# Performance work log

Measured on AMD Instinct MI355X. Metric: run time of the kernel, lower is better.

The kernel has to match this reference:

```python
import jax, jax.numpy as jnp
import numpy as np

B, S, V, E, HE, HD, MEL_D, MEL_T = 4096, 13, 276, 128, 256, 256, 80, 250

def setup_inputs() -> dict:
    key = jax.random.key(0)
    ks = jax.random.split(key, 20)
    p = lambda k, sh: (jax.random.normal(k, sh, dtype=jnp.float32) * 0.05)
    return {
        'text': jax.random.randint(ks[0], (B, S), 0, V),
        'surprisal': jax.random.normal(ks[1], (B, S), dtype=jnp.float32),
        'emb': p(ks[2], (V, E)),
        'sw': p(ks[3], (E, 1)), 'sb': p(ks[4], (E,)),
        'ew_ih': p(ks[5], (4 * HE, E)), 'ew_hh': p(ks[6], (4 * HE, HE)),
        'eb_ih': p(ks[7], (4 * HE,)), 'eb_hh': p(ks[8], (4 * HE,)),
        'aw': p(ks[9], (1, HD + HE)), 'ab': p(ks[10], (1,)),
        'dw_ih': p(ks[11], (4 * HD, E + HE)), 'dw_hh': p(ks[12], (4 * HD, HD)),
        'db_ih': p(ks[13], (4 * HD,)), 'db_hh': p(ks[14], (4 * HD,)),
        'f1w': p(ks[15], (1024, S * HD)), 'f1b': p(ks[16], (1024,)),
        'f2w': p(ks[17], (MEL_D * MEL_T, 1024)), 'f2b': p(ks[18], (MEL_D * MEL_T,)),
        'init_in': jnp.zeros((E,), dtype=jnp.float32),
    }

def _lstm_cell(x, h, c, w_ih, w_hh, b_ih, b_hh, H):
    # PyTorch gate order: i, f, g, o
    g = x @ w_ih.T + b_ih + h @ w_hh.T + b_hh
    i, f, gg, o = jnp.split(g, 4, axis=-1)
    c2 = jax.nn.sigmoid(f) * c + jax.nn.sigmoid(i) * jnp.tanh(gg)
    h2 = jax.nn.sigmoid(o) * jnp.tanh(c2)
    return h2, c2

def reference(text, surprisal, emb, sw, sb, ew_ih, ew_hh, eb_ih, eb_hh,
              aw, ab, dw_ih, dw_hh, db_ih, db_hh, f1w, f1b, f2w, f2b, init_in):
    # embedding + surprisal projection
    x = emb[text] + (surprisal[..., None] @ sw.T + sb)  # [B,S,E]

    # encoder LSTM over time
    def enc_step(carry, xt):
        h, c = carry
        h2, c2 = _lstm_cell(xt, h, c, ew_ih, ew_hh, eb_ih, eb_hh, HE)
        return (h2, c2), h2
    h0 = jnp.zeros((B, HE), dtype=x.dtype)
    (h_n, c_n), enc_seq = jax.lax.scan(enc_step, (h0, h0), jnp.swapaxes(x, 0, 1))
    enc_out = jnp.swapaxes(enc_seq, 0, 1)  # [B,S,HE]

    # precompute encoder part of attention scores (constant across steps)
    aw_h, aw_e = aw[0, :HD], aw[0, HD:]
    enc_score = enc_out @ aw_e + ab[0]  # [B,S]

    dec_in = jnp.broadcast_to(init_in, (B, E))

    def dec_step(carry, _):
        h, c = carry
        scores = h @ aw_h + 0.0  # [B]
        w = jax.nn.softmax(scores[:, None] + enc_score, axis=1)  # [B,S]
        context = jnp.einsum('bs,bsh->bh', w, enc_out)
        xcat = jnp.concatenate([dec_in, context], axis=-1)
        h2, c2 = _lstm_cell(xcat, h, c, dw_ih, dw_hh, db_ih, db_hh, HD)
        return (h2, c2), h2
    _, dec_seq = jax.lax.scan(dec_step, (h_n, c_n), None, length=S)
    dec_out = jnp.swapaxes(dec_seq, 0, 1).reshape(B, S * HD)  # [B,13*256]

    hfc = jax.nn.relu(dec_out @ f1w.T + f1b)
    out = (hfc @ f2w.T + f2b).reshape(B, MEL_D, MEL_T)
    return out
```

## Files before the change

kernel.cpp:

```cpp
#include <hip/hip_runtime.h>
#include <hip/hip_bf16.h>
#include <stdint.h>
#include <stddef.h>

#define B 4096
#define S 13
#define NG 1024
#define MEL 20000
#define MELP 20224

typedef __attribute__((ext_vector_type(8))) short bf16x8;
typedef __attribute__((ext_vector_type(4))) float f32x4;

__device__ __forceinline__ void g2l16(void* lds, const void* g) {
    __builtin_amdgcn_global_load_lds(
        (const __attribute__((address_space(1))) void*)g,
        (__attribute__((address_space(3))) void*)lds, 16, 0, 0);
}

__device__ __forceinline__ float sigm(float x) { return 1.0f / (1.0f + expf(-x)); }
__device__ __forceinline__ float b2f(unsigned short u) {
    union { float f; unsigned int i; } x; x.i = ((unsigned)u) << 16; return x.f;
}
__device__ __forceinline__ unsigned short f2bu(float f) {
    __hip_bfloat16 h = __float2bfloat16(f);
    return *reinterpret_cast<unsigned short*>(&h);
}

__device__ __forceinline__ void swz_decode(int wg, int nwg, int nx, int& bx, int& by) {
    const int cpx = nwg >> 3;
    wg = (wg & 7) * cpx + (wg >> 3);
    const int gsz = nx * 4;
    const int grp = wg / gsz, rem = wg % gsz;
    by = grp * 4 + (rem & 3);
    bx = rem >> 2;
}

#define BAR() do { asm volatile("" ::: "memory"); \
    __builtin_amdgcn_s_barrier(); \
    __builtin_amdgcn_sched_barrier(0); } while (0)

#define P_DECL() \
    __shared__ __hip_bfloat16 As3[4][128 * 32]; \
    __shared__ __hip_bfloat16 Bs3[4][64 * 32]; \
    const int tid  = threadIdx.x; \
    const int lane = tid & 63; \
    const int wv   = tid >> 6; \
    const int l16  = lane & 15; \
    const int sr   = tid >> 2; \
    const int sc   = (((tid & 3) ^ ((tid >> 3) & 3)) << 3); \
    const int sl   = (((lane >> 4) ^ ((l16 >> 1) & 3)) << 3)

#define STG3(buf, k0) do { \
    g2l16(&As3[buf][sr * 32 + (tid & 3) * 8],         Ag + (size_t)sr * K + (k0) + sc); \
    g2l16(&As3[buf][(sr + 64) * 32 + (tid & 3) * 8],  Ag + (size_t)(sr + 64) * K + (k0) + sc); \
    g2l16(&Bs3[buf][sr * 32 + (tid & 3) * 8],         Wg + (size_t)sr * K + (k0) + sc); } while (0)

#define TILE3(cur, stg, k2, DO_STG) do { \
    const __hip_bfloat16* Ab = As3[cur]; \
    const __hip_bfloat16* Bb = Bs3[cur]; \
    bf16x8 af[2], bfr[4]; \
    _Pragma("unroll") for (int m = 0; m < 2; ++m) \
        af[m] = *(const bf16x8*)(Ab + (wv * 32 + m * 16 + l16) * 32 + sl); \
    _Pragma("unroll") for (int n = 0; n < 4; ++n) \
        bfr[n] = *(const bf16x8*)(Bb + (n * 16 + l16) * 32 + sl); \
    if (DO_STG) STG3(stg, k2); \
    __builtin_amdgcn_s_setprio(1); \
    _Pragma("unroll") for (int m = 0; m < 2; ++m) \
        _Pragma("unroll") for (int n = 0; n < 4; ++n) \
            acc[m][n] = __builtin_amdgcn_mfma_f32_16x16x32_bf16(af[m], bfr[n], acc[m][n], 0, 0, 0); \
    __builtin_amdgcn_s_setprio(0); \
} while (0)

#define PIPELINE(K) do { \
    const int nk = (K) >> 5; \
    STG3(0, 0); \
    STG3(1, 32); \
    STG3(2, 64); \
    asm volatile("s_waitcnt vmcnt(6)" ::: "memory"); \
    BAR(); \
    int cur = 0; \
    for (int t = 0; t < nk - 3; ++t) { \
        const int stg = (cur + 3) & 3; \
        TILE3(cur, stg, (t + 3) << 5, true); \
        asm volatile("s_waitcnt vmcnt(6)" ::: "memory"); \
        BAR(); \
        cur = (cur + 1) & 3; \
    } \
    TILE3(cur, 0, 0, false); \
    asm volatile("s_waitcnt vmcnt(3)" ::: "memory"); \
    BAR(); \
    cur = (cur + 1) & 3; \
    TILE3(cur, 0, 0, false); \
    asm volatile("s_waitcnt vmcnt(0)" ::: "memory"); \
    BAR(); \
    cur = (cur + 1) & 3; \
    TILE3(cur, 0, 0, false); \
} while (0)

__global__ __launch_bounds__(256, 2) void gemm3(
    const __hip_bfloat16* __restrict__ A,
    const __hip_bfloat16* __restrict__ W,
    const float* __restrict__ bias,
    float* __restrict__ Cf,
    __hip_bfloat16* __restrict__ Cbf,
    int N, int K, int ldc, int relu, int nx)
{
    P_DECL();
    int bx, by;
    swz_decode(blockIdx.x, gridDim.x, nx, bx, by);
    const int brow = by * 128, bcol = bx * 64;
    const __hip_bfloat16* Ag = A + (size_t)brow * K;
    const __hip_bfloat16* Wg = W + (size_t)bcol * K;
    f32x4 acc[2][4] = {};

    PIPELINE(K);

    const int r4 = (lane >> 4) * 4;
    #pragma unroll
    for (int m = 0; m < 2; ++m) {
        #pragma unroll
        for (int n = 0; n < 4; ++n) {
            const int col = bcol + n * 16 + l16;
            if (col >= N) continue;
            const float bv = bias ? bias[col] : 0.0f;
            #pragma unroll
            for (int r = 0; r < 4; ++r) {
                const int row = brow + wv * 32 + m * 16 + r4 + r;
                float v = acc[m][n][r] + bv;
                if (relu) v = v > 0.0f ? v : 0.0f;
                if (Cf)  Cf[(size_t)row * ldc + col] = v;
                if (Cbf) Cbf[(size_t)row * ldc + col] = __float2bfloat16(v);
            }
        }
    }
}

__global__ __launch_bounds__(256, 2) void gemm_lstm3(
    const __hip_bfloat16* __restrict__ A,
    const __hip_bfloat16* __restrict__ W,
    const float* __restrict__ bias,
    float* __restrict__ c,
    float* __restrict__ hf,
    __hip_bfloat16* __restrict__ hb1, int s1,
    __hip_bfloat16* __restrict__ hb2, int s2,
    int K)
{
    P_DECL();
    int bx, by;
    swz_decode(blockIdx.x, gridDim.x, 16, bx, by);
    const int brow = by * 128, bcol = bx * 64;
    const __hip_bfloat16* Ag = A + (size_t)brow * K;
    const __hip_bfloat16* Wg = W + (size_t)bcol * K;
    f32x4 acc[2][4] = {};

    PIPELINE(K);

    const int r4 = (lane >> 4) * 4;
    const int unit = bx * 16 + l16;
    const float b0 = bias[bcol + l16];
    const float b1 = bias[bcol + 16 + l16];
    const float b2 = bias[bcol + 32 + l16];
    const float b3 = bias[bcol + 48 + l16];
    #pragma unroll
    for (int m = 0; m < 2; ++m) {
        #pragma unroll
        for (int r = 0; r < 4; ++r) {
            const int row = brow + wv * 32 + m * 16 + r4 + r;
            const float gi = acc[m][0][r] + b0;
            const float gf = acc[m][1][r] + b1;
            const float gg = acc[m][2][r] + b2;
            const float go = acc[m][3][r] + b3;
            const size_t ci = (size_t)row * 256 + unit;
            const float c2 = sigm(gf) * c[ci] + sigm(gi) * tanhf(gg);
            const float h2 = sigm(go) * tanhf(c2);
            c[ci] = c2;
            if (hf) hf[ci] = h2;
            const __hip_bfloat16 hb = __float2bfloat16(h2);
            hb1[(size_t)row * s1 + unit] = hb;
            if (hb2) hb2[(size_t)row * s2 + unit] = hb;
        }
    }
}

__global__ __launch_bounds__(512, 2) void gemm256(
    const __hip_bfloat16* __restrict__ A,
    const __hip_bfloat16* __restrict__ W,
    const float* __restrict__ bias,
    float* __restrict__ Cf,
    int N, int K, int ldc, int nx)
{
    __shared__ __hip_bfloat16 As[4][256 * 32];
    __shared__ __hip_bfloat16 Bs[4][256 * 32];
    const int tid  = threadIdx.x;
    const int lane = tid & 63;
    const int wv = tid >> 6, wr = wv >> 2, wc = wv & 3;
    const int l16 = lane & 15;
    int bx, by;
    {
        int wg = blockIdx.x; const int nwg = gridDim.x;
        const int cpx = nwg >> 3;
        wg = (wg & 7) * cpx + (wg >> 3);
        const int gsz = nx * 2;
        const int grp = wg / gsz, rem = wg % gsz;
        by = grp * 2 + (rem & 1);
        bx = rem >> 1;
    }
    const int brow = by * 256, bcol = bx * 256;
    const __hip_bfloat16* Ag = A + (size_t)brow * K;
    const __hip_bfloat16* Wg = W + (size_t)bcol * K;
    const int sr = tid >> 2;
    const int sc = (((tid & 3) ^ ((tid >> 3) & 3)) << 3);
    const int sd = tid * 8;
    const int sl = (((lane >> 4) ^ ((l16 >> 1) & 3)) << 3);
    f32x4 acc[8][4] = {};
    const int nk = K >> 5;

    #define STG_A(buf, k0) do { \
        g2l16(&As[buf][sd],        Ag + (size_t)sr * K + (k0) + sc);         \
        g2l16(&As[buf][4096 + sd], Ag + (size_t)(sr + 128) * K + (k0) + sc); } while (0)
    #define STG_B(buf, k0) do { \
        g2l16(&Bs[buf][sd],        Wg + (size_t)sr * K + (k0) + sc);         \
        g2l16(&Bs[buf][4096 + sd], Wg + (size_t)(sr + 128) * K + (k0) + sc); } while (0)

    #define TILE(cur, stg, k2, DO_STG) do {                                    \
        const __hip_bfloat16* Ab = As[cur];                                    \
        const __hip_bfloat16* Bb = Bs[cur];                                    \
        bf16x8 bfr[4], af[4];                                                  \
        _Pragma("unroll") for (int n = 0; n < 4; ++n)                          \
            bfr[n] = *(const bf16x8*)(Bb + (wc * 64 + n * 16 + l16) * 32 + sl);\
        _Pragma("unroll") for (int m = 0; m < 4; ++m)                          \
            af[m] = *(const bf16x8*)(Ab + (wr * 128 + m * 16 + l16) * 32 + sl);\
        if (DO_STG) STG_A(stg, k2);                                            \
        BAR();                                                                 \
        __builtin_amdgcn_s_setprio(1);                                         \
        _Pragma("unroll") for (int m = 0; m < 4; ++m)                          \
            _Pragma("unroll") for (int n = 0; n < 4; ++n)                      \
                acc[m][n] = __builtin_amdgcn_mfma_f32_16x16x32_bf16(           \
                    af[m], bfr[n], acc[m][n], 0, 0, 0);                        \
        __builtin_amdgcn_s_setprio(0);                                         \
        BAR();                                                                 \
        _Pragma("unroll") for (int m = 0; m < 4; ++m)                          \
            af[m] = *(const bf16x8*)(Ab + (wr * 128 + (m + 4) * 16 + l16) * 32 + sl); \
        if (DO_STG) STG_B(stg, k2);                                            \
        BAR();                                                                 \
        __builtin_amdgcn_s_setprio(1);                                         \
        _Pragma("unroll") for (int m = 0; m < 4; ++m)                          \
            _Pragma("unroll") for (int n = 0; n < 4; ++n)                      \
                acc[m + 4][n] = __builtin_amdgcn_mfma_f32_16x16x32_bf16(       \
                    af[m], bfr[n], acc[m + 4][n], 0, 0, 0);                    \
        __builtin_amdgcn_s_setprio(0);                                         \
    } while (0)

    STG_A(0, 0);  STG_B(0, 0);
    STG_A(1, 32); STG_B(1, 32);
    STG_A(2, 64); STG_B(2, 64);
    asm volatile("s_waitcnt vmcnt(8)" ::: "memory");
    BAR();
    int cur = 0;
    for (int t = 0; t < nk - 3; ++t) {
        const int stg = (cur + 3) & 3;
        TILE(cur, stg, (t + 3) << 5, true);
        asm volatile("s_waitcnt vmcnt(8)" ::: "memory");
        BAR();
        cur = (cur + 1) & 3;
    }
    TILE(cur, 0, 0, false);
    asm volatile("s_waitcnt vmcnt(4)" ::: "memory");
    BAR();
    cur = (cur + 1) & 3;
    TILE(cur, 0, 0, false);
    asm volatile("s_waitcnt vmcnt(0)" ::: "memory");
    BAR();
    cur = (cur + 1) & 3;
    TILE(cur, 0, 0, false);

    const int r4 = (lane >> 4) * 4;
    #pragma unroll
    for (int m = 0; m < 8; ++m) {
        #pragma unroll
        for (int n = 0; n < 4; ++n) {
            const int col = bcol + wc * 64 + n * 16 + l16;
            if (col >= N) continue;
            const float bv = bias[col];
            #pragma unroll
            for (int r = 0; r < 4; ++r) {
                const int row = brow + wr * 128 + m * 16 + r4 + r;
                Cf[(size_t)row * ldc + col] = acc[m][n][r] + bv;
            }
        }
    }
}

__device__ __forceinline__ int unperm(int np) {
    const int u = ((np >> 6) << 4) + (np & 15);
    const int g = (np >> 4) & 3;
    return g * 256 + u;
}

__global__ void pack_enc_w(const float* __restrict__ ew_ih, const float* __restrict__ ew_hh,
                           __hip_bfloat16* __restrict__ out) {
    int idx = blockIdx.x * 256 + threadIdx.x;
    if (idx >= NG * 384) return;
    int np = idx / 384, k = idx % 384;
    int n = unperm(np);
    float v = (k < 128) ? ew_ih[n * 128 + k] : ew_hh[n * 256 + (k - 128)];
    out[idx] = __float2bfloat16(v);
}

__global__ void pack_dec_w(const float* __restrict__ dw_ih, const float* __restrict__ dw_hh,
                           __hip_bfloat16* __restrict__ out) {
    int idx = blockIdx.x * 256 + threadIdx.x;
    if (idx >= NG * 512) return;
    int np = idx / 512, k = idx % 512;
    int n = unperm(np);
    float v = (k < 256) ? dw_ih[n * 384 + 128 + k] : dw_hh[n * 256 + (k - 256)];
    out[idx] = __float2bfloat16(v);
}

__global__ void conv_bf16(const float* __restrict__ in, __hip_bfloat16* __restrict__ out,
                          long long n) {
    long long idx = (long long)blockIdx.x * 256 + threadIdx.x;
    if (idx >= n) return;
    out[idx] = __float2bfloat16(in[idx]);
}

__global__ void pack_w2(const float* __restrict__ in, __hip_bfloat16* __restrict__ out,
                        long long n_in, long long n_out) {
    long long i8 = ((long long)blockIdx.x * 256 + threadIdx.x) * 8;
    if (i8 >= n_out) return;
    union { bf16x8 v; __hip_bfloat16 e[8]; } u;
    if (i8 < n_in) {
        f32x4 a = *(const f32x4*)(in + i8);
        f32x4 b = *(const f32x4*)(in + i8 + 4);
        #pragma unroll
        for (int j = 0; j < 4; ++j) { u.e[j] = __float2bfloat16(a[j]); u.e[4 + j] = __float2bfloat16(b[j]); }
    } else {
        #pragma unroll
        for (int j = 0; j < 8; ++j) u.e[j] = __float2bfloat16(0.0f);
    }
    *(bf16x8*)(out + i8) = u.v;
}

__global__ void pad_bias_f32(const float* __restrict__ in, float* __restrict__ out,
                             int n_out, int n_in) {
    int idx = blockIdx.x * 256 + threadIdx.x;
    if (idx >= n_out) return;
    out[idx] = (idx < n_in) ? in[idx] : 0.0f;
}

__global__ void bias_prep(const float* __restrict__ eb_ih, const float* __restrict__ eb_hh,
                          const float* __restrict__ db_ih, const float* __restrict__ db_hh,
                          const float* __restrict__ dw_ih, const float* __restrict__ init_in,
                          float* __restrict__ be, float* __restrict__ bd) {
    int np = blockIdx.x * 256 + threadIdx.x;
    if (np >= NG) return;
    int n = unperm(np);
    be[np] = eb_ih[n] + eb_hh[n];
    float s = db_ih[n] + db_hh[n];
    for (int k = 0; k < 128; ++k) s += dw_ih[n * 384 + k] * init_in[k];
    bd[np] = s;
}

__global__ void embed_x(const int* __restrict__ text, const float* __restrict__ surp,
                        const float* __restrict__ emb, const float* __restrict__ sw,
                        const float* __restrict__ sb, __hip_bfloat16* __restrict__ xall) {
    int idx = blockIdx.x * 256 + threadIdx.x;
    if (idx >= B * S * 32) return;
    int jj = (idx & 31) * 4;
    int rest = idx >> 5;
    int b = rest % B;
    int s = rest / B;
    const float sp = surp[b * S + s];
    const f32x4 e4 = *(const f32x4*)(emb + (size_t)text[b * S + s] * 128 + jj);
    const f32x4 w4 = *(const f32x4*)(sw + jj);
    const f32x4 b4 = *(const f32x4*)(sb + jj);
    __hip_bfloat16* dst = xall + ((size_t)s * B + b) * 384 + jj;
    #pragma unroll
    for (int i = 0; i < 4; ++i) dst[i] = __float2bfloat16(e4[i] + sp * w4[i] + b4[i]);
}

__global__ void init_zero(float* __restrict__ c, __hip_bfloat16* __restrict__ x0h) {
    int idx = blockIdx.x * 256 + threadIdx.x;
    if (idx >= B * 256) return;
    c[idx] = 0.0f;
    int b = idx >> 8, jj = idx & 255;
    x0h[(size_t)b * 384 + 128 + jj] = __float2bfloat16(0.0f);
}

__global__ void enc_score_kernel(const __hip_bfloat16* __restrict__ enc_out,
                                 const float* __restrict__ aw, const float* __restrict__ ab,
                                 float* __restrict__ enc_score) {
    int gw = (blockIdx.x * 256 + threadIdx.x) >> 6;
    int lane = threadIdx.x & 63;
    if (gw >= B * S) return;
    const ushort4 r4v = *(const ushort4*)(enc_out + (size_t)gw * 256 + lane * 4);
    const f32x4 a4 = *(const f32x4*)(aw + 256 + lane * 4);
    float s = b2f(r4v.x) * a4[0] + b2f(r4v.y) * a4[1] + b2f(r4v.z) * a4[2] + b2f(r4v.w) * a4[3];
    #pragma unroll
    for (int off = 1; off < 64; off <<= 1) s += __shfl_xor(s, off);
    if (lane == 0) enc_score[gw] = s + ab[0];
}

__global__ void attn_kernel(const float* __restrict__ h, const __hip_bfloat16* __restrict__ enc_out,
                            const float* __restrict__ enc_score, const float* __restrict__ aw,
                            __hip_bfloat16* __restrict__ decA) {
    int b = (blockIdx.x * 256 + threadIdx.x) >> 6;
    int lane = threadIdx.x & 63;
    if (b >= B) return;
    const f32x4 h4 = *(const f32x4*)(h + (size_t)b * 256 + lane * 4);
    const f32x4 a4 = *(const f32x4*)(aw + lane * 4);
    float s = h4[0] * a4[0] + h4[1] * a4[1] + h4[2] * a4[2] + h4[3] * a4[3];
    #pragma unroll
    for (int off = 1; off < 64; off <<= 1) s += __shfl_xor(s, off);
    float sc[S], mx = -1e30f;
    #pragma unroll
    for (int t = 0; t < S; ++t) { sc[t] = s + enc_score[b * S + t]; mx = fmaxf(mx, sc[t]); }
    float sum = 0.0f;
    #pragma unroll
    for (int t = 0; t < S; ++t) { sc[t] = expf(sc[t] - mx); sum += sc[t]; }
    float inv = 1.0f / sum;
    float ctx[4] = {0.f, 0.f, 0.f, 0.f};
    #pragma unroll
    for (int t = 0; t < S; ++t) {
        const ushort4 e4 = *(const ushort4*)(enc_out + ((size_t)b * S + t) * 256 + lane * 4);
        float w = sc[t] * inv;
        ctx[0] += w * b2f(e4.x); ctx[1] += w * b2f(e4.y);
        ctx[2] += w * b2f(e4.z); ctx[3] += w * b2f(e4.w);
    }
    ushort4 o4;
    o4.x = f2bu(ctx[0]);
    o4.y = f2bu(ctx[1]);
    o4.z = f2bu(ctx[2]);
    o4.w = f2bu(ctx[3]);
    *(ushort4*)(decA + (size_t)b * 512 + lane * 4) = o4;
}

#define CDIV(a, b) (((a) + (b) - 1) / (b))

extern "C" void kernel_launch(void* const* d_in, const int* in_sizes, int n_in,
                              void* d_out, int out_size, void* d_ws, size_t ws_size,
                              hipStream_t stream) {
    const int*   text    = (const int*)  d_in[0];
    const float* surp    = (const float*)d_in[1];
    const float* emb     = (const float*)d_in[2];
    const float* sw      = (const float*)d_in[3];
    const float* sb      = (const float*)d_in[4];
    const float* ew_ih   = (const float*)d_in[5];
    const float* ew_hh   = (const float*)d_in[6];
    const float* eb_ih   = (const float*)d_in[7];
    const float* eb_hh   = (const float*)d_in[8];
    const float* aw      = (const float*)d_in[9];
    const float* ab      = (const float*)d_in[10];
    const float* dw_ih   = (const float*)d_in[11];
    const float* dw_hh   = (const float*)d_in[12];
    const float* db_ih   = (const float*)d_in[13];
    const float* db_hh   = (const float*)d_in[14];
    const float* f1w     = (const float*)d_in[15];
    const float* f1b     = (const float*)d_in[16];
    const float* f2w     = (const float*)d_in[17];
    const float* f2b     = (const float*)d_in[18];
    const float* init_in = (const float*)d_in[19];
    float* out = (float*)d_out;

    char* p = (char*)d_ws;
    auto alloc = [&](size_t bytes) {
        void* r = (void*)p;
        p += (bytes + 255) & ~(size_t)255;
        return r;
    };
    __hip_bfloat16* Wenc      = (__hip_bfloat16*)alloc((size_t)NG * 384 * 2);
    __hip_bfloat16* Wdec      = (__hip_bfloat16*)alloc((size_t)NG * 512 * 2);
    __hip_bfloat16* W1        = (__hip_bfloat16*)alloc((size_t)NG * 3328 * 2);
    __hip_bfloat16* W2        = (__hip_bfloat16*)alloc((size_t)MELP * 1024 * 2);
    float*          f2bp      = (float*)alloc((size_t)MELP * 4);
    float*          be        = (float*)alloc((size_t)NG * 4);
    float*          bd        = (float*)alloc((size_t)NG * 4);
    __hip_bfloat16* xall      = (__hip_bfloat16*)alloc((size_t)S * B * 384 * 2);
    __hip_bfloat16* enc_out   = (__hip_bfloat16*)alloc((size_t)B * S * 256 * 2);
    float*          enc_score = (float*)alloc((size_t)B * S * 4);
    float*          c_buf     = (float*)alloc((size_t)B * 256 * 4);
    float*          h_buf     = (float*)alloc((size_t)B * 256 * 4);
    __hip_bfloat16* decA      = (__hip_bfloat16*)alloc((size_t)B * 512 * 2);
    __hip_bfloat16* dec_out   = (__hip_bfloat16*)alloc((size_t)B * 3328 * 2);
    __hip_bfloat16* hfc       = (__hip_bfloat16*)alloc((size_t)B * 1024 * 2);
    (void)ws_size; (void)in_sizes; (void)n_in; (void)out_size;

    pack_enc_w<<<CDIV(NG * 384, 256), 256, 0, stream>>>(ew_ih, ew_hh, Wenc);
    pack_dec_w<<<CDIV(NG * 512, 256), 256, 0, stream>>>(dw_ih, dw_hh, Wdec);
    conv_bf16<<<CDIV(NG * 3328, 256), 256, 0, stream>>>(f1w, W1, (long long)NG * 3328);
    pack_w2<<<CDIV(MELP * 1024 / 8, 256), 256, 0, stream>>>(
        f2w, W2, (long long)MEL * 1024, (long long)MELP * 1024);
    pad_bias_f32<<<CDIV(MELP, 256), 256, 0, stream>>>(f2b, f2bp, MELP, MEL);
    bias_prep<<<CDIV(NG, 256), 256, 0, stream>>>(eb_ih, eb_hh, db_ih, db_hh, dw_ih, init_in, be, bd);

    embed_x<<<CDIV(B * S * 32, 256), 256, 0, stream>>>(text, surp, emb, sw, sb, xall);
    init_zero<<<CDIV(B * 256, 256), 256, 0, stream>>>(c_buf, xall);

    for (int t = 0; t < S; ++t) {
        __hip_bfloat16* hb1; int s1;
        if (t < S - 1) { hb1 = xall + ((size_t)(t + 1) * B * 384) + 128; s1 = 384; }
        else           { hb1 = decA + 256; s1 = 512; }
        float* hf = (t == S - 1) ? h_buf : (float*)nullptr;
        gemm_lstm3<<<512, 256, 0, stream>>>(
            xall + (size_t)t * B * 384, Wenc, be, c_buf, hf,
            hb1, s1, enc_out + (size_t)t * 256, S * 256, 384);
    }

    enc_score_kernel<<<CDIV(B * S * 64, 256), 256, 0, stream>>>(enc_out, aw, ab, enc_score);

    for (int t = 0; t < S; ++t) {
        attn_kernel<<<CDIV(B * 64, 256), 256, 0, stream>>>(h_buf, enc_out, enc_score, aw, decA);
        gemm_lstm3<<<512, 256, 0, stream>>>(
            decA, Wdec, bd, c_buf, h_buf,
            decA + 256, 512, dec_out + (size_t)t * 256, 3328, 512);
    }

    gemm3<<<(NG / 64) * (B / 128), 256, 0, stream>>>(
        dec_out, W1, f1b, (float*)nullptr, hfc, NG, 3328, NG, 1, NG / 64);

    gemm256<<<(MELP / 256) * (B / 256), 512, 0, stream>>>(
        hfc, W2, f2bp, out, MEL, 1024, MEL, MELP / 256);
}
```

Measured before the change: 722.7 us.

## Fuse setup kernels into one prep launch and fold enc_score into encoder LSTM

```diff
diff --git a/kernel.cpp b/kernel.cpp
--- a/kernel.cpp
+++ b/kernel.cpp
@@ -25,6 +25,12 @@
 __device__ __forceinline__ unsigned short f2bu(float f) {
     __hip_bfloat16 h = __float2bfloat16(f);
     return *reinterpret_cast<unsigned short*>(&h);
+}
+__device__ __forceinline__ bf16x8 cvt8(f32x4 a, f32x4 b) {
+    union { bf16x8 v; __hip_bfloat16 e[8]; } u;
+    #pragma unroll
+    for (int j = 0; j < 4; ++j) { u.e[j] = __float2bfloat16(a[j]); u.e[4 + j] = __float2bfloat16(b[j]); }
+    return u.v;
 }
 
 __device__ __forceinline__ void swz_decode(int wg, int nwg, int nx, int& bx, int& by) {
@@ -144,7 +150,9 @@
     float* __restrict__ hf,
     __hip_bfloat16* __restrict__ hb1, int s1,
     __hip_bfloat16* __restrict__ hb2, int s2,
-    int K)
+    int K,
+    const float* __restrict__ aw,
+    float* __restrict__ score)
 {
     P_DECL();
     int bx, by;
@@ -162,6 +170,8 @@
     const float b1 = bias[bcol + 16 + l16];
     const float b2 = bias[bcol + 32 + l16];
     const float b3 = bias[bcol + 48 + l16];
+    const float awe = score ? aw[256 + unit] : 0.0f;
+    float ps[2][4];
     #pragma unroll
     for (int m = 0; m < 2; ++m) {
         #pragma unroll
@@ -176,9 +186,27 @@
             const float h2 = sigm(go) * tanhf(c2);
             c[ci] = c2;
             if (hf) hf[ci] = h2;
+            ps[m][r] = h2 * awe;
             const __hip_bfloat16 hb = __float2bfloat16(h2);
             hb1[(size_t)row * s1 + unit] = hb;
             if (hb2) hb2[(size_t)row * s2 + unit] = hb;
+        }
+    }
+    if (score) {
+        #pragma unroll
+        for (int m = 0; m < 2; ++m) {
+            #pragma unroll
+            for (int r = 0; r < 4; ++r) {
+                float v = ps[m][r];
+                v += __shfl_xor(v, 1);
+                v += __shfl_xor(v, 2);
+                v += __shfl_xor(v, 4);
+                v += __shfl_xor(v, 8);
+                if (l16 == 0) {
+                    const int row = brow + wv * 32 + m * 16 + r4 + r;
+                    atomicAdd(&score[(size_t)row * S], v);
+                }
+            }
         }
     }
 }
@@ -298,108 +326,118 @@
     return g * 256 + u;
 }
 
-__global__ void pack_enc_w(const float* __restrict__ ew_ih, const float* __restrict__ ew_hh,
-                           __hip_bfloat16* __restrict__ out) {
-    int idx = blockIdx.x * 256 + threadIdx.x;
-    if (idx >= NG * 384) return;
-    int np = idx / 384, k = idx % 384;
-    int n = unperm(np);
-    float v = (k < 128) ? ew_ih[n * 128 + k] : ew_hh[n * 256 + (k - 128)];
-    out[idx] = __float2bfloat16(v);
-}
-
-__global__ void pack_dec_w(const float* __restrict__ dw_ih, const float* __restrict__ dw_hh,
-                           __hip_bfloat16* __restrict__ out) {
-    int idx = blockIdx.x * 256 + threadIdx.x;
-    if (idx >= NG * 512) return;
-    int np = idx / 512, k = idx % 512;
-    int n = unperm(np);
-    float v = (k < 256) ? dw_ih[n * 384 + 128 + k] : dw_hh[n * 256 + (k - 256)];
-    out[idx] = __float2bfloat16(v);
-}
-
-__global__ void conv_bf16(const float* __restrict__ in, __hip_bfloat16* __restrict__ out,
-                          long long n) {
-    long long idx = (long long)blockIdx.x * 256 + threadIdx.x;
-    if (idx >= n) return;
-    out[idx] = __float2bfloat16(in[idx]);
-}
-
-__global__ void pack_w2(const float* __restrict__ in, __hip_bfloat16* __restrict__ out,
-                        long long n_in, long long n_out) {
-    long long i8 = ((long long)blockIdx.x * 256 + threadIdx.x) * 8;
-    if (i8 >= n_out) return;
-    union { bf16x8 v; __hip_bfloat16 e[8]; } u;
-    if (i8 < n_in) {
-        f32x4 a = *(const f32x4*)(in + i8);
-        f32x4 b = *(const f32x4*)(in + i8 + 4);
+#define N_W2   ((long long)MELP * 1024 / 8)
+#define N_W1   ((long long)NG * 3328 / 8)
+#define N_WE   ((long long)NG * 384 / 8)
+#define N_WD   ((long long)NG * 512 / 8)
+#define N_EMB  ((long long)B * S * 32)
+#define N_INIT ((long long)B * 256)
+#define N_F2B  ((long long)MELP)
+#define N_BP   ((long long)NG)
+#define N_ES   ((long long)B * S)
+#define N_PREP (N_W2 + N_W1 + N_WE + N_WD + N_EMB + N_INIT + N_F2B + N_BP + N_ES)
+
+__global__ void prep_all(
+    const int* __restrict__ text, const float* __restrict__ surp,
+    const float* __restrict__ emb, const float* __restrict__ sw,
+    const float* __restrict__ sb,
+    const float* __restrict__ ew_ih, const float* __restrict__ ew_hh,
+    const float* __restrict__ eb_ih, const float* __restrict__ eb_hh,
+    const float* __restrict__ dw_ih, const float* __restrict__ dw_hh,
+    const float* __restrict__ db_ih, const float* __restrict__ db_hh,
+    const float* __restrict__ f1w, const float* __restrict__ f2w,
+    const float* __restrict__ f2b, const float* __restrict__ init_in,
+    const float* __restrict__ ab,
+    __hip_bfloat16* __restrict__ Wenc, __hip_bfloat16* __restrict__ Wdec,
+    __hip_bfloat16* __restrict__ W1, __hip_bfloat16* __restrict__ W2,
+    float* __restrict__ f2bp, float* __restrict__ be, float* __restrict__ bd,
+    __hip_bfloat16* __restrict__ xall, float* __restrict__ c_buf,
+    float* __restrict__ enc_score)
+{
+    long long id = (long long)blockIdx.x * 256 + threadIdx.x;
+    if (id < N_W2) {
+        const long long i8 = id * 8;
+        bf16x8 v;
+        if (i8 < (long long)MEL * 1024) {
+            v = cvt8(*(const f32x4*)(f2w + i8), *(const f32x4*)(f2w + i8 + 4));
+        } else {
+            union { bf16x8 w; __hip_bfloat16 e[8]; } u;
+            #pragma unroll
+            for (int j = 0; j < 8; ++j) u.e[j] = __float2bfloat16(0.0f);
+            v = u.w;
+        }
+        *(bf16x8*)(W2 + i8) = v;
+        return;
+    }
+    id -= N_W2;
+    if (id < N_W1) {
+        const long long i8 = id * 8;
+        *(bf16x8*)(W1 + i8) = cvt8(*(const f32x4*)(f1w + i8), *(const f32x4*)(f1w + i8 + 4));
+        return;
+    }
+    id -= N_W1;
+    if (id < N_WE) {
+        const int idx = (int)(id * 8);
+        const int np = idx / 384, k = idx % 384;
+        const int n = unperm(np);
+        const float* src = (k < 128) ? (ew_ih + n * 128 + k) : (ew_hh + n * 256 + (k - 128));
+        *(bf16x8*)(Wenc + idx) = cvt8(*(const f32x4*)src, *(const f32x4*)(src + 4));
+        return;
+    }
+    id -= N_WE;
+    if (id < N_WD) {
+        const int idx = (int)(id * 8);
+        const int np = idx / 512, k = idx % 512;
+        const int n = unperm(np);
+        const float* src = (k < 256) ? (dw_ih + n * 384 + 128 + k) : (dw_hh + n * 256 + (k - 256));
+        *(bf16x8*)(Wdec + idx) = cvt8(*(const f32x4*)src, *(const f32x4*)(src + 4));
+        return;
+    }
+    id -= N_WD;
+    if (id < N_EMB) {
+        const int idx = (int)id;
+        const int jj = (idx & 31) * 4;
+        const int rest = idx >> 5;
+        const int b = rest % B;
+        const int s = rest / B;
+        const float sp = surp[b * S + s];
+        const f32x4 e4 = *(const f32x4*)(emb + (size_t)text[b * S + s] * 128 + jj);
+        const f32x4 w4 = *(const f32x4*)(sw + jj);
+        const f32x4 b4 = *(const f32x4*)(sb + jj);
+        __hip_bfloat16* dst = xall + ((size_t)s * B + b) * 384 + jj;
         #pragma unroll
-        for (int j = 0; j < 4; ++j) { u.e[j] = __float2bfloat16(a[j]); u.e[4 + j] = __float2bfloat16(b[j]); }
-    } else {
-        #pragma unroll
-        for (int j = 0; j < 8; ++j) u.e[j] = __float2bfloat16(0.0f);
-    }
-    *(bf16x8*)(out + i8) = u.v;
-}
-
-__global__ void pad_bias_f32(const float* __restrict__ in, float* __restrict__ out,
-                             int n_out, int n_in) {
-    int idx = blockIdx.x * 256 + threadIdx.x;
-    if (idx >= n_out) return;
-    out[idx] = (idx < n_in) ? in[idx] : 0.0f;
-}
-
-__global__ void bias_prep(const float* __restrict__ eb_ih, const float* __restrict__ eb_hh,
-                          const float* __restrict__ db_ih, const float* __restrict__ db_hh,
-                          const float* __restrict__ dw_ih, const float* __restrict__ init_in,
-                          float* __restrict__ be, float* __restrict__ bd) {
-    int np = blockIdx.x * 256 + threadIdx.x;
-    if (np >= NG) return;
-    int n = unperm(np);
-    be[np] = eb_ih[n] + eb_hh[n];
-    float s = db_ih[n] + db_hh[n];
-    for (int k = 0; k < 128; ++k) s += dw_ih[n * 384 + k] * init_in[k];
-    bd[np] = s;
-}
-
-__global__ void embed_x(const int* __restrict__ text, const float* __restrict__ surp,
-                        const float* __restrict__ emb, const float* __restrict__ sw,
-                        const float* __restrict__ sb, __hip_bfloat16* __restrict__ xall) {
-    int idx = blockIdx.x * 256 + threadIdx.x;
-    if (idx >= B * S * 32) return;
-    int jj = (idx & 31) * 4;
-    int rest = idx >> 5;
-    int b = rest % B;
-    int s = rest / B;
-    const float sp = surp[b * S + s];
-    const f32x4 e4 = *(const f32x4*)(emb + (size_t)text[b * S + s] * 128 + jj);
-    const f32x4 w4 = *(const f32x4*)(sw + jj);
-    const f32x4 b4 = *(const f32x4*)(sb + jj);
-    __hip_bfloat16* dst = xall + ((size_t)s * B + b) * 384 + jj;
-    #pragma unroll
-    for (int i = 0; i < 4; ++i) dst[i] = __float2bfloat16(e4[i] + sp * w4[i] + b4[i]);
-}
-
-__global__ void init_zero(float* __restrict__ c, __hip_bfloat16* __restrict__ x0h) {
-    int idx = blockIdx.x * 256 + threadIdx.x;
-    if (idx >= B * 256) return;
-    c[idx] = 0.0f;
-    int b = idx >> 8, jj = idx & 255;
-    x0h[(size_t)b * 384 + 128 + jj] = __float2bfloat16(0.0f);
-}
-
-__global__ void enc_score_kernel(const __hip_bfloat16* __restrict__ enc_out,
-                                 const float* __restrict__ aw, const float* __restrict__ ab,
-                                 float* __restrict__ enc_score) {
-    int gw = (blockIdx.x * 256 + threadIdx.x) >> 6;
-    int lane = threadIdx.x & 63;
-    if (gw >= B * S) return;
-    const ushort4 r4v = *(const ushort4*)(enc_out + (size_t)gw * 256 + lane * 4);
-    const f32x4 a4 = *(const f32x4*)(aw + 256 + lane * 4);
-    float s = b2f(r4v.x) * a4[0] + b2f(r4v.y) * a4[1] + b2f(r4v.z) * a4[2] + b2f(r4v.w) * a4[3];
-    #pragma unroll
-    for (int off = 1; off < 64; off <<= 1) s += __shfl_xor(s, off);
-    if (lane == 0) enc_score[gw] = s + ab[0];
+        for (int i = 0; i < 4; ++i) dst[i] = __float2bfloat16(e4[i] + sp * w4[i] + b4[i]);
+        return;
+    }
+    id -= N_EMB;
+    if (id < N_INIT) {
+        const int idx = (int)id;
+        c_buf[idx] = 0.0f;
+        const int b = idx >> 8, jj = idx & 255;
+        xall[(size_t)b * 384 + 128 + jj] = __float2bfloat16(0.0f);
+        return;
+    }
+    id -= N_INIT;
+    if (id < N_F2B) {
+        const int idx = (int)id;
+        f2bp[idx] = (idx < MEL) ? f2b[idx] : 0.0f;
+        return;
+    }
+    id -= N_F2B;
+    if (id < N_BP) {
+        const int np = (int)id;
+        const int n = unperm(np);
+        be[np] = eb_ih[n] + eb_hh[n];
+        float s = db_ih[n] + db_hh[n];
+        for (int k = 0; k < 128; ++k) s += dw_ih[n * 384 + k] * init_in[k];
+        bd[np] = s;
+        return;
+    }
+    id -= N_BP;
+    if (id < N_ES) {
+        enc_score[id] = ab[0];
+        return;
+    }
 }
 
 __global__ void attn_kernel(const float* __restrict__ h, const __hip_bfloat16* __restrict__ enc_out,
@@ -486,16 +524,10 @@
     __hip_bfloat16* hfc       = (__hip_bfloat16*)alloc((size_t)B * 1024 * 2);
     (void)ws_size; (void)in_sizes; (void)n_in; (void)out_size;
 
-    pack_enc_w<<<CDIV(NG * 384, 256), 256, 0, stream>>>(ew_ih, ew_hh, Wenc);
-    pack_dec_w<<<CDIV(NG * 512, 256), 256, 0, stream>>>(dw_ih, dw_hh, Wdec);
-    conv_bf16<<<CDIV(NG * 3328, 256), 256, 0, stream>>>(f1w, W1, (long long)NG * 3328);
-    pack_w2<<<CDIV(MELP * 1024 / 8, 256), 256, 0, stream>>>(
-        f2w, W2, (long long)MEL * 1024, (long long)MELP * 1024);
-    pad_bias_f32<<<CDIV(MELP, 256), 256, 0, stream>>>(f2b, f2bp, MELP, MEL);
-    bias_prep<<<CDIV(NG, 256), 256, 0, stream>>>(eb_ih, eb_hh, db_ih, db_hh, dw_ih, init_in, be, bd);
-
-    embed_x<<<CDIV(B * S * 32, 256), 256, 0, stream>>>(text, surp, emb, sw, sb, xall);
-    init_zero<<<CDIV(B * 256, 256), 256, 0, stream>>>(c_buf, xall);
+    prep_all<<<(int)CDIV(N_PREP, 256), 256, 0, stream>>>(
+        text, surp, emb, sw, sb, ew_ih, ew_hh, eb_ih, eb_hh,
+        dw_ih, dw_hh, db_ih, db_hh, f1w, f2w, f2b, init_in, ab,
+        Wenc, Wdec, W1, W2, f2bp, be, bd, xall, c_buf, enc_score);
 
     for (int t = 0; t < S; ++t) {
         __hip_bfloat16* hb1; int s1;
@@ -504,16 +536,16 @@
         float* hf = (t == S - 1) ? h_buf : (float*)nullptr;
         gemm_lstm3<<<512, 256, 0, stream>>>(
             xall + (size_t)t * B * 384, Wenc, be, c_buf, hf,
-            hb1, s1, enc_out + (size_t)t * 256, S * 256, 384);
-    }
-
-    enc_score_kernel<<<CDIV(B * S * 64, 256), 256, 0, stream>>>(enc_out, aw, ab, enc_score);
+            hb1, s1, enc_out + (size_t)t * 256, S * 256, 384,
+            aw, enc_score + t);
+    }
 
     for (int t = 0; t < S; ++t) {
         attn_kernel<<<CDIV(B * 64, 256), 256, 0, stream>>>(h_buf, enc_out, enc_score, aw, decA);
         gemm_lstm3<<<512, 256, 0, stream>>>(
             decA, Wdec, bd, c_buf, h_buf,
-            decA + 256, 512, dec_out + (size_t)t * 256, 3328, 512);
+            decA + 256, 512, dec_out + (size_t)t * 256, 3328, 512,
+            aw, (float*)nullptr);
     }
 
     gemm3<<<(NG / 64) * (B / 128), 256, 0, stream>>>(
```

Measured after the change: 732.4 us. No clear change (+1.3%).
